# Performance work log

Measured on AMD Instinct MI355X. Metric: run time of the kernel, lower is better.

Reference implementation:

```python
import math
import jax, jax.numpy as jnp
import numpy as np

B, S, H, NH = 4, 2048, 1024, 16
HD = H // NH  # 64


def _rope_cos_sin(seq_len, dim, base=10000.0):
    # freqs[j] = base^(-2j/dim), angles = outer(t, freqs)
    inv = 1.0 / (base ** (jnp.arange(0, dim, 2, dtype=jnp.float32) / dim))
    t = jnp.arange(seq_len, dtype=jnp.float32)
    ang = jnp.outer(t, inv)  # (S, dim//2)
    return jnp.cos(ang), jnp.sin(ang)


def _apply_rope(x, cos, sin):
    # x: (B, S, NH, HD); pairs are (x[2i], x[2i+1]) per torch view_as_complex on reshape(..., -1, 2)
    xr = x.reshape(*x.shape[:-1], HD // 2, 2)
    x0, x1 = xr[..., 0], xr[..., 1]
    c = cos[None, :, None, :]  # (1, S, 1, HD//2)
    s = sin[None, :, None, :]
    o0 = x0 * c - x1 * s
    o1 = x0 * s + x1 * c
    return jnp.stack([o0, o1], axis=-1).reshape(x.shape)


def setup_inputs() -> dict:
    key = jax.random.key(0)
    ks = jax.random.split(key, 5)
    scale = 1.0 / math.sqrt(H)
    return {
        "x": jax.random.normal(ks[0], (B, S, H), dtype=jnp.float32),
        "wq": jax.random.normal(ks[1], (H, H), dtype=jnp.float32) * scale,
        "wk": jax.random.normal(ks[2], (H, H), dtype=jnp.float32) * scale,
        "wv": jax.random.normal(ks[3], (H, H), dtype=jnp.float32) * scale,
        "wo": jax.random.normal(ks[4], (H, H), dtype=jnp.float32) * scale,
        "attention_mask": jnp.ones((B, S), dtype=jnp.int32),
    }


def reference(x, wq, wk, wv, wo, attention_mask):
    # Linear(bias=False): y = x @ W.T with W shape (out, in)
    q = jnp.einsum('bsh,oh->bso', x, wq).reshape(B, S, NH, HD)
    k = jnp.einsum('bsh,oh->bso', x, wk).reshape(B, S, NH, HD)
    v = jnp.einsum('bsh,oh->bso', x, wv).reshape(B, S, NH, HD)
    cos, sin = _rope_cos_sin(S, HD)
    q = _apply_rope(q, cos, sin)
    k = _apply_rope(k, cos, sin)
    # scores: (B, NH, S, S)
    scores = jnp.einsum('bqhd,bkhd->bhqk', q, k) / math.sqrt(HD)
    mask = attention_mask[:, None, None, :]  # (B,1,1,S)
    scores = jnp.where(mask == 0, -jnp.inf, scores)
    attn = jax.nn.softmax(scores, axis=-1)
    # attn_dropout: eval mode / p=0 -> identity
    out = jnp.einsum('bhqk,bkhd->bqhd', attn, v).reshape(B, S, H)
    return jnp.einsum('bsh,oh->bso', out, wo)
```

## Files before the change

### kernel.cpp

```cpp
#include <hip/hip_runtime.h>
#include <hip/hip_bf16.h>

#define B_   4
#define S_   2048
#define H_   1024
#define NH_  16
#define HD_  64
#define M_   8192
#define K_   1024

using bf16x8 = __bf16 __attribute__((ext_vector_type(8)));
using f32x4  = float __attribute__((ext_vector_type(4)));
using f32x16 = float __attribute__((ext_vector_type(16)));

__device__ inline f32x4 mfma16(bf16x8 a, bf16x8 b, f32x4 c) {
    return __builtin_amdgcn_mfma_f32_16x16x32_bf16(a, b, c, 0, 0, 0);
}
__device__ inline f32x16 mfma32(bf16x8 a, bf16x8 b, f32x16 c) {
    return __builtin_amdgcn_mfma_f32_32x32x16_bf16(a, b, c, 0, 0, 0);
}

__device__ inline unsigned short f2bf(float f) {
    __hip_bfloat16 h = __float2bfloat16(f);
    return *reinterpret_cast<unsigned short*>(&h);
}

__device__ inline unsigned cvt_pk_bf16(float lo, float hi) {
    unsigned r;
    asm("v_cvt_pk_bf16_f32 %0, %1, %2" : "=v"(r) : "v"(lo), "v"(hi));
    return r;
}

__device__ inline void perm32swap(unsigned &a, unsigned &b) {
    asm("v_permlane32_swap_b32 %0, %1" : "+v"(a), "+v"(b));
}

__device__ inline void gload_lds16(const unsigned short* g, unsigned short* l) {
    __builtin_amdgcn_global_load_lds(
        (const __attribute__((address_space(1))) void*)g,
        (__attribute__((address_space(3))) void*)l, 16, 0, 0);
}

#define EXP2F(x) __builtin_amdgcn_exp2f(x)


__global__ __launch_bounds__(256) void prep_convert(
    const float* __restrict__ x,  const float* __restrict__ wq,
    const float* __restrict__ wk, const float* __restrict__ wv,
    const float* __restrict__ wo, unsigned short* __restrict__ ws)
{
    size_t u = (size_t)blockIdx.x * 256 + threadIdx.x;
    const float* src; unsigned short* dst; size_t off;
    if (u < 2097152)      { src = x;  dst = ws;            off = u * 4; }
    else if (u < 2359296) { src = wq; dst = ws + 8388608;  off = (u - 2097152) * 4; }
    else if (u < 2621440) { src = wk; dst = ws + 9437184;  off = (u - 2359296) * 4; }
    else if (u < 2883584) { src = wv; dst = ws + 10485760; off = (u - 2621440) * 4; }
    else                  { src = wo; dst = ws + 11534336; off = (u - 2883584) * 4; }
    float4 v = *reinterpret_cast<const float4*>(src + off);
    ushort4 o;
    o.x = f2bf(v.x); o.y = f2bf(v.y); o.z = f2bf(v.z); o.w = f2bf(v.w);
    *reinterpret_cast<ushort4*>(dst + off) = o;
}

__global__ __launch_bounds__(256) void rope_table(
    float* __restrict__ cosb, float* __restrict__ sinb,
    const int* __restrict__ mask, float* __restrict__ biasb)
{
    int idx = blockIdx.x * 256 + threadIdx.x;
    int pos = idx >> 5, i = idx & 31;
    float inv = expf(-(float)(2 * i) * (9.210340371976184f / 64.0f));
    float ang = (float)pos * inv;
    cosb[idx] = cosf(ang);
    sinb[idx] = sinf(ang);
    if (idx < B_ * S_)
        biasb[idx] = mask[idx] ? -12.0f : -__builtin_inff();
}

__global__ __launch_bounds__(256) void gemm_qkv(
    const unsigned short* __restrict__ A,
    const unsigned short* __restrict__ W,
    unsigned short* __restrict__ qbuf, unsigned short* __restrict__ kbuf,
    unsigned short* __restrict__ vtb,
    const float* __restrict__ cosb, const float* __restrict__ sinb)
{
    __shared__ alignas(16) unsigned short Al[128 * 64];
    __shared__ alignas(16) unsigned short Bl[128 * 64];

    const int t = threadIdx.x;
    const int l = t & 63;
    const int w = t >> 6;
    const int lane_r = l & 15, lane_g = l >> 4;
    const int bn = blockIdx.x, bm = blockIdx.y;
    const size_t rowbase = (size_t)bm * 128;
    const int colbase = bn * 128;
    const int wm = (w >> 1) * 64, wn = (w & 1) * 64;
    const int which = colbase >> 10;
    const float scale = (which == 0) ? 0.18033688089184827f : 1.0f;

    const int glrow  = l >> 3;
    const int glslot = (l & 7) ^ glrow;

    f32x4 zero4 = {0.f, 0.f, 0.f, 0.f};
    f32x4 acc[4][4];
#pragma unroll
    for (int a = 0; a < 4; a++)
#pragma unroll
        for (int b2 = 0; b2 < 4; b2++) acc[a][b2] = zero4;

    for (int k0 = 0; k0 < K_; k0 += 64) {
#pragma unroll
        for (int i = 0; i < 4; i++) {
            int rbase = i * 32 + w * 8;
            int row = rbase + glrow;
            gload_lds16(A + (rowbase + row) * K_ + k0 + glslot * 8, &Al[rbase * 64]);
            gload_lds16(W + (size_t)(colbase + row) * K_ + k0 + glslot * 8, &Bl[rbase * 64]);
        }
        __syncthreads();

        bf16x8 af[4][2], bfr[4][2];
#pragma unroll
        for (int mt = 0; mt < 4; mt++)
#pragma unroll
            for (int kk = 0; kk < 2; kk++) {
                int rowa = wm + mt * 16 + lane_r;
                int offa = (rowa * 128 + kk * 64 + lane_g * 16) ^ ((rowa & 7) << 4);
                af[mt][kk] = *reinterpret_cast<const bf16x8*>((const char*)Al + offa);
                int rowb = wn + mt * 16 + lane_r;
                int offb = (rowb * 128 + kk * 64 + lane_g * 16) ^ ((rowb & 7) << 4);
                bfr[mt][kk] = *reinterpret_cast<const bf16x8*>((const char*)Bl + offb);
            }
#pragma unroll
        for (int mt = 0; mt < 4; mt++)
#pragma unroll
            for (int nt = 0; nt < 4; nt++) {
                acc[mt][nt] = mfma16(af[mt][0], bfr[nt][0], acc[mt][nt]);
                acc[mt][nt] = mfma16(af[mt][1], bfr[nt][1], acc[mt][nt]);
            }
        __syncthreads();
    }

#pragma unroll
    for (int mt = 0; mt < 4; mt++) {
#pragma unroll
        for (int nt = 0; nt < 4; nt++) {
            if (which <= 1) {
                unsigned short* out = which ? kbuf : qbuf;
#pragma unroll
                for (int i = 0; i < 4; i++) {
                    size_t r = rowbase + wm + mt * 16 + lane_g * 4 + i;
                    int n = (colbase & 1023) + wn + nt * 16 + lane_r;
                    int b   = (int)(r >> 11);
                    int pos = (int)(r & 2047);
                    int h = n >> 6, d = n & 63;
                    float cv = cosb[pos * 32 + (d >> 1)];
                    float sv = sinb[pos * 32 + (d >> 1)];
                    float val = acc[mt][nt][i];
                    float partner = __shfl_xor(val, 1);
                    float o = (d & 1) ? (partner * sv + val * cv)
                                      : (val * cv - partner * sv);
                    o *= scale;
                    out[(((size_t)(b * NH_ + h)) * S_ + pos) * 64 + d] = f2bf(o);
                }
            } else {
                unsigned short* out = vtb;
                size_t rr = rowbase + wm + mt * 16 + lane_g * 4;
                int n = (colbase & 1023) + wn + nt * 16 + lane_r;
                int b   = (int)(rr >> 11);
                int pos = (int)(rr & 2047);
                int h = n >> 6, d = n & 63;
                ushort4 o;
                o.x = f2bf(acc[mt][nt][0]); o.y = f2bf(acc[mt][nt][1]);
                o.z = f2bf(acc[mt][nt][2]); o.w = f2bf(acc[mt][nt][3]);
                *reinterpret_cast<ushort4*>(
                    out + (((size_t)(b * NH_ + h)) * 64 + d) * S_ + pos) = o;
            }
        }
    }
}

__global__ __launch_bounds__(256) void gemm_wo(
    const unsigned short* __restrict__ A,
    const unsigned short* __restrict__ W,
    float* __restrict__ out)
{
    __shared__ alignas(16) unsigned short Al[128 * 64];
    __shared__ alignas(16) unsigned short Bl[128 * 64];

    const int t = threadIdx.x;
    const int l = t & 63;
    const int w = t >> 6;
    const int lane_r = l & 15, lane_g = l >> 4;
    const int bn = blockIdx.x, bm = blockIdx.y;
    const size_t rowbase = (size_t)bm * 128;
    const int colbase = bn * 128;
    const int wm = (w >> 1) * 64, wn = (w & 1) * 64;

    const int glrow  = l >> 3;
    const int glslot = (l & 7) ^ glrow;

    f32x4 zero4 = {0.f, 0.f, 0.f, 0.f};
    f32x4 acc[4][4];
#pragma unroll
    for (int a = 0; a < 4; a++)
#pragma unroll
        for (int b2 = 0; b2 < 4; b2++) acc[a][b2] = zero4;

    for (int k0 = 0; k0 < K_; k0 += 64) {
#pragma unroll
        for (int i = 0; i < 4; i++) {
            int rbase = i * 32 + w * 8;
            int row = rbase + glrow;
            gload_lds16(A + (rowbase + row) * K_ + k0 + glslot * 8, &Al[rbase * 64]);
            gload_lds16(W + (size_t)(colbase + row) * K_ + k0 + glslot * 8, &Bl[rbase * 64]);
        }
        __syncthreads();

        bf16x8 af[4][2], bfr[4][2];
#pragma unroll
        for (int mt = 0; mt < 4; mt++)
#pragma unroll
            for (int kk = 0; kk < 2; kk++) {
                int rowa = wm + mt * 16 + lane_r;
                int offa = (rowa * 128 + kk * 64 + lane_g * 16) ^ ((rowa & 7) << 4);
                af[mt][kk] = *reinterpret_cast<const bf16x8*>((const char*)Al + offa);
                int rowb = wn + mt * 16 + lane_r;
                int offb = (rowb * 128 + kk * 64 + lane_g * 16) ^ ((rowb & 7) << 4);
                bfr[mt][kk] = *reinterpret_cast<const bf16x8*>((const char*)Bl + offb);
            }
#pragma unroll
        for (int mt = 0; mt < 4; mt++)
#pragma unroll
            for (int nt = 0; nt < 4; nt++) {
                acc[mt][nt] = mfma16(af[mt][0], bfr[nt][0], acc[mt][nt]);
                acc[mt][nt] = mfma16(af[mt][1], bfr[nt][1], acc[mt][nt]);
            }
        __syncthreads();
    }

#pragma unroll
    for (int mt = 0; mt < 4; mt++)
#pragma unroll
        for (int nt = 0; nt < 4; nt++)
#pragma unroll
            for (int i = 0; i < 4; i++) {
                size_t r = rowbase + wm + mt * 16 + lane_g * 4 + i;
                int n = colbase + wn + nt * 16 + lane_r;
                out[r * 1024 + n] = acc[mt][nt][i];
            }
}

__global__ __launch_bounds__(256, 2) void attn_fwd(
    const unsigned short* __restrict__ qb, const unsigned short* __restrict__ kb,
    const unsigned short* __restrict__ vt, const float* __restrict__ biasb,
    unsigned short* __restrict__ ao)
{
    __shared__ alignas(16) unsigned short Kl[2][64 * 64];
    __shared__ alignas(16) unsigned short Vl[2][64 * 64];

    const int bid = blockIdx.x;
    const int xcd = bid & 7, idx = bid >> 3;
    const int bh = xcd * 8 + (idx >> 3);
    const int qt = idx & 7;
    const int b = bh >> 4, h = bh & 15;

    const int t = threadIdx.x, l = t & 63, w = t >> 6;
    const int lr = l & 31;
    const int hi = l >> 5;
    const int row8 = lr & 7;

    const unsigned short* qp = qb + (size_t)bh * S_ * 64;
    const unsigned short* kp = kb + (size_t)bh * S_ * 64;
    const unsigned short* vp = vt + (size_t)bh * 64 * S_;
    const float* bp = biasb + (size_t)b * S_;

    bf16x8 qf[2][4];
#pragma unroll
    for (int qbk = 0; qbk < 2; qbk++) {
        int qrow = qt * 256 + w * 64 + qbk * 32 + lr;
#pragma unroll
        for (int ks = 0; ks < 4; ks++)
            qf[qbk][ks] = *reinterpret_cast<const bf16x8*>(
                qp + (size_t)qrow * 64 + ks * 16 + hi * 8);
    }

    f32x16 oacc[2][2];
#pragma unroll
    for (int qbk = 0; qbk < 2; qbk++)
#pragma unroll
        for (int r = 0; r < 16; r++) { oacc[qbk][0][r] = 0.f; oacc[qbk][1][r] = 0.f; }
    float lsum[2] = {0.f, 0.f};

    const int grr = l >> 3;
    const int gss = ((l & 7) ^ grr) * 8;

#define STAGE(bi, kt)                                                          \
    {                                                                          \
        _Pragma("unroll")                                                      \
        for (int c = 0; c < 2; c++) {                                          \
            int rbase = w * 16 + c * 8;                                        \
            gload_lds16(kp + (size_t)((kt) * 64 + rbase + grr) * 64 + gss,     \
                        &Kl[bi][rbase * 64]);                                  \
            gload_lds16(vp + (size_t)(rbase + grr) * S_ + (kt) * 64 + gss,     \
                        &Vl[bi][rbase * 64]);                                  \
        }                                                                      \
    }

    STAGE(0, 0)

    for (int kt = 0; kt < 32; kt++) {
        const int cur = kt & 1;
        __syncthreads();
        if (kt < 31) STAGE(cur ^ 1, kt + 1)

        f32x16 sacc[2][2];
#pragma unroll
        for (int T = 0; T < 2; T++) {
#pragma unroll
            for (int g = 0; g < 4; g++) {
                float4 bv = *reinterpret_cast<const float4*>(
                    bp + kt * 64 + T * 32 + g * 8 + hi * 4);
                sacc[0][T][g * 4 + 0] = bv.x; sacc[0][T][g * 4 + 1] = bv.y;
                sacc[0][T][g * 4 + 2] = bv.z; sacc[0][T][g * 4 + 3] = bv.w;
            }
            sacc[1][T] = sacc[0][T];
        }

        __builtin_amdgcn_s_setprio(1);
#pragma unroll
        for (int T = 0; T < 2; T++) {
            int rowb = (32 * T + lr) * 128;
#pragma unroll
            for (int ks = 0; ks < 4; ks++) {
                bf16x8 kf = *reinterpret_cast<const bf16x8*>(
                    (const char*)Kl[cur] + rowb + (((2 * ks + hi) ^ row8) << 4));
                sacc[0][T] = mfma32(kf, qf[0][ks], sacc[0][T]);
                sacc[1][T] = mfma32(kf, qf[1][ks], sacc[1][T]);
            }
        }
        __builtin_amdgcn_s_setprio(0);

        bf16x8 pa[2][4];
#pragma unroll
        for (int qbk = 0; qbk < 2; qbk++) {
            unsigned u[2][8];
            float r0 = 0.f, r1 = 0.f, r2 = 0.f, r3 = 0.f;
#pragma unroll
            for (int T = 0; T < 2; T++) {
                float p[16];
#pragma unroll
                for (int r = 0; r < 16; r++) p[r] = EXP2F(sacc[qbk][T][r]);
#pragma unroll
                for (int r = 0; r < 16; r += 4) {
                    r0 += p[r]; r1 += p[r + 1]; r2 += p[r + 2]; r3 += p[r + 3];
                }
#pragma unroll
                for (int bq = 0; bq < 4; bq++) {
                    u[T][bq * 2 + 0] = cvt_pk_bf16(p[bq * 4 + 0], p[bq * 4 + 1]);
                    u[T][bq * 2 + 1] = cvt_pk_bf16(p[bq * 4 + 2], p[bq * 4 + 3]);
                }
            }
            lsum[qbk] += (r0 + r1) + (r2 + r3);
#pragma unroll
            for (int ks = 0; ks < 4; ks++) {
                int T = ks >> 1, e = ks & 1;
                unsigned a0 = u[T][4 * e + 0], b0 = u[T][4 * e + 2];
                unsigned a1 = u[T][4 * e + 1], b1 = u[T][4 * e + 3];
                perm32swap(a0, b0);
                perm32swap(a1, b1);
                unsigned q4[4] = {a0, a1, b0, b1};
                pa[qbk][ks] = *reinterpret_cast<const bf16x8*>(q4);
            }
        }

        __builtin_amdgcn_s_setprio(1);
#pragma unroll
        for (int dt = 0; dt < 2; dt++) {
            int rowb = (32 * dt + lr) * 128;
#pragma unroll
            for (int ks = 0; ks < 4; ks++) {
                bf16x8 vf = *reinterpret_cast<const bf16x8*>(
                    (const char*)Vl[cur] + rowb + (((2 * ks + hi) ^ row8) << 4));
                oacc[0][dt] = mfma32(vf, pa[0][ks], oacc[0][dt]);
                oacc[1][dt] = mfma32(vf, pa[1][ks], oacc[1][dt]);
            }
        }
        __builtin_amdgcn_s_setprio(0);
    }
#undef STAGE

#pragma unroll
    for (int qbk = 0; qbk < 2; qbk++) {
        float ls = lsum[qbk];
        ls += __shfl_xor(ls, 32);
        float rl = 1.0f / ls;
        size_t obase = ((size_t)(b * S_) + qt * 256 + w * 64 + qbk * 32 + lr) * 1024 + h * 64;
#pragma unroll
        for (int dt = 0; dt < 2; dt++)
#pragma unroll
            for (int g = 0; g < 4; g++) {
                uint2 o;
                o.x = cvt_pk_bf16(oacc[qbk][dt][g * 4 + 0] * rl, oacc[qbk][dt][g * 4 + 1] * rl);
                o.y = cvt_pk_bf16(oacc[qbk][dt][g * 4 + 2] * rl, oacc[qbk][dt][g * 4 + 3] * rl);
                *reinterpret_cast<uint2*>(ao + obase + 32 * dt + 8 * g + 4 * hi) = o;
            }
    }
}

extern "C" void kernel_launch(void* const* d_in, const int* in_sizes, int n_in,
                              void* d_out, int out_size, void* d_ws, size_t ws_size,
                              hipStream_t stream)
{
    const float* x  = (const float*)d_in[0];
    const float* wq = (const float*)d_in[1];
    const float* wk = (const float*)d_in[2];
    const float* wv = (const float*)d_in[3];
    const float* wo = (const float*)d_in[4];
    const int* mask = (const int*)d_in[5];

    unsigned short* ws   = (unsigned short*)d_ws;
    unsigned short* xb   = ws;
    unsigned short* wqkv = ws + 8388608;
    unsigned short* wob  = ws + 11534336;
    unsigned short* qbuf = ws + 12582912;
    unsigned short* kbuf = ws + 20971520;
    unsigned short* vtb  = ws + 29360128;
    float* cosb  = (float*)(ws + 37748736);
    float* sinb  = cosb + 65536;
    float* biasb = sinb + 65536;
    unsigned short* aob = xb;

    prep_convert<<<12288, 256, 0, stream>>>(x, wq, wk, wv, wo, ws);
    rope_table<<<256, 256, 0, stream>>>(cosb, sinb, mask, biasb);

    gemm_qkv<<<dim3(24, 64), 256, 0, stream>>>(xb, wqkv, qbuf, kbuf, vtb, cosb, sinb);

    attn_fwd<<<512, 256, 0, stream>>>(qbuf, kbuf, vtb, biasb, aob);

    gemm_wo<<<dim3(8, 64), 256, 0, stream>>>(aob, wob, (float*)d_out);
}
```

Before: 203.7 us.

## Transpose QK MFMA operands for vectorized RoPE epilogue, interleave cos/sin, prefetch bias

```diff
diff --git a/kernel.cpp b/kernel.cpp
--- a/kernel.cpp
+++ b/kernel.cpp
@@ -63,15 +63,15 @@
 }
 
 __global__ __launch_bounds__(256) void rope_table(
-    float* __restrict__ cosb, float* __restrict__ sinb,
-    const int* __restrict__ mask, float* __restrict__ biasb)
+    float2* __restrict__ ropeb, const int* __restrict__ mask,
+    float* __restrict__ biasb)
 {
     int idx = blockIdx.x * 256 + threadIdx.x;
     int pos = idx >> 5, i = idx & 31;
     float inv = expf(-(float)(2 * i) * (9.210340371976184f / 64.0f));
     float ang = (float)pos * inv;
-    cosb[idx] = cosf(ang);
-    sinb[idx] = sinf(ang);
+    float2 cs; cs.x = cosf(ang); cs.y = sinf(ang);
+    ropeb[idx] = cs;
     if (idx < B_ * S_)
         biasb[idx] = mask[idx] ? -12.0f : -__builtin_inff();
 }
@@ -81,7 +81,7 @@
     const unsigned short* __restrict__ W,
     unsigned short* __restrict__ qbuf, unsigned short* __restrict__ kbuf,
     unsigned short* __restrict__ vtb,
-    const float* __restrict__ cosb, const float* __restrict__ sinb)
+    const float* __restrict__ ropeb)
 {
     __shared__ alignas(16) unsigned short Al[128 * 64];
     __shared__ alignas(16) unsigned short Bl[128 * 64];
@@ -129,52 +129,68 @@
                 int offb = (rowb * 128 + kk * 64 + lane_g * 16) ^ ((rowb & 7) << 4);
                 bfr[mt][kk] = *reinterpret_cast<const bf16x8*>((const char*)Bl + offb);
             }
-#pragma unroll
-        for (int mt = 0; mt < 4; mt++)
-#pragma unroll
-            for (int nt = 0; nt < 4; nt++) {
-                acc[mt][nt] = mfma16(af[mt][0], bfr[nt][0], acc[mt][nt]);
-                acc[mt][nt] = mfma16(af[mt][1], bfr[nt][1], acc[mt][nt]);
-            }
+        if (which <= 1) {
+#pragma unroll
+            for (int a = 0; a < 4; a++)
+#pragma unroll
+                for (int b2 = 0; b2 < 4; b2++) {
+                    acc[a][b2] = mfma16(bfr[a][0], af[b2][0], acc[a][b2]);
+                    acc[a][b2] = mfma16(bfr[a][1], af[b2][1], acc[a][b2]);
+                }
+        } else {
+#pragma unroll
+            for (int a = 0; a < 4; a++)
+#pragma unroll
+                for (int b2 = 0; b2 < 4; b2++) {
+                    acc[a][b2] = mfma16(af[a][0], bfr[b2][0], acc[a][b2]);
+                    acc[a][b2] = mfma16(af[a][1], bfr[b2][1], acc[a][b2]);
+                }
+        }
         __syncthreads();
     }
 
-#pragma unroll
-    for (int mt = 0; mt < 4; mt++) {
-#pragma unroll
-        for (int nt = 0; nt < 4; nt++) {
-            if (which <= 1) {
-                unsigned short* out = which ? kbuf : qbuf;
-#pragma unroll
-                for (int i = 0; i < 4; i++) {
-                    size_t r = rowbase + wm + mt * 16 + lane_g * 4 + i;
-                    int n = (colbase & 1023) + wn + nt * 16 + lane_r;
-                    int b   = (int)(r >> 11);
-                    int pos = (int)(r & 2047);
-                    int h = n >> 6, d = n & 63;
-                    float cv = cosb[pos * 32 + (d >> 1)];
-                    float sv = sinb[pos * 32 + (d >> 1)];
-                    float val = acc[mt][nt][i];
-                    float partner = __shfl_xor(val, 1);
-                    float o = (d & 1) ? (partner * sv + val * cv)
-                                      : (val * cv - partner * sv);
-                    o *= scale;
-                    out[(((size_t)(b * NH_ + h)) * S_ + pos) * 64 + d] = f2bf(o);
-                }
-            } else {
-                unsigned short* out = vtb;
-                size_t rr = rowbase + wm + mt * 16 + lane_g * 4;
-                int n = (colbase & 1023) + wn + nt * 16 + lane_r;
-                int b   = (int)(rr >> 11);
+    if (which <= 1) {
+        unsigned short* out = which ? kbuf : qbuf;
+#pragma unroll
+        for (int a = 0; a < 4; a++) {
+            int nbase = (colbase & 1023) + wn + a * 16 + 4 * lane_g;
+            int h = nbase >> 6, d0 = nbase & 63;
+#pragma unroll
+            for (int b2 = 0; b2 < 4; b2++) {
+                size_t r = rowbase + wm + b2 * 16 + lane_r;
+                int bb  = (int)(r >> 11);
+                int pos = (int)(r & 2047);
+                float4 cs = *reinterpret_cast<const float4*>(
+                    ropeb + pos * 64 + d0);
+                float a0 = acc[a][b2][0], a1 = acc[a][b2][1];
+                float a2 = acc[a][b2][2], a3 = acc[a][b2][3];
+                float o0 = (a0 * cs.x - a1 * cs.y) * scale;
+                float o1 = (a0 * cs.y + a1 * cs.x) * scale;
+                float o2 = (a2 * cs.z - a3 * cs.w) * scale;
+                float o3 = (a2 * cs.w + a3 * cs.z) * scale;
+                uint2 o;
+                o.x = cvt_pk_bf16(o0, o1);
+                o.y = cvt_pk_bf16(o2, o3);
+                *reinterpret_cast<uint2*>(
+                    out + (((size_t)(bb * NH_ + h)) * S_ + pos) * 64 + d0) = o;
+            }
+        }
+    } else {
+#pragma unroll
+        for (int a = 0; a < 4; a++)
+#pragma unroll
+            for (int b2 = 0; b2 < 4; b2++) {
+                size_t rr = rowbase + wm + a * 16 + lane_g * 4;
+                int n = (colbase & 1023) + wn + b2 * 16 + lane_r;
+                int bb  = (int)(rr >> 11);
                 int pos = (int)(rr & 2047);
                 int h = n >> 6, d = n & 63;
                 ushort4 o;
-                o.x = f2bf(acc[mt][nt][0]); o.y = f2bf(acc[mt][nt][1]);
-                o.z = f2bf(acc[mt][nt][2]); o.w = f2bf(acc[mt][nt][3]);
+                o.x = f2bf(acc[a][b2][0]); o.y = f2bf(acc[a][b2][1]);
+                o.z = f2bf(acc[a][b2][2]); o.w = f2bf(acc[a][b2][3]);
                 *reinterpret_cast<ushort4*>(
-                    out + (((size_t)(b * NH_ + h)) * 64 + d) * S_ + pos) = o;
-            }
-        }
+                    vtb + (((size_t)(bb * NH_ + h)) * 64 + d) * S_ + pos) = o;
+            }
     }
 }
 
@@ -305,7 +321,19 @@
         }                                                                      \
     }
 
+#define LOADBIAS(kt)                                                           \
+    {                                                                          \
+        _Pragma("unroll")                                                      \
+        for (int T = 0; T < 2; T++)                                            \
+            _Pragma("unroll")                                                  \
+            for (int g = 0; g < 4; g++)                                        \
+                bvreg[T * 4 + g] = *reinterpret_cast<const float4*>(           \
+                    bp + (kt) * 64 + T * 32 + g * 8 + hi * 4);                 \
+    }
+
+    float4 bvreg[8];
     STAGE(0, 0)
+    LOADBIAS(0)
 
     for (int kt = 0; kt < 32; kt++) {
         const int cur = kt & 1;
@@ -314,16 +342,16 @@
 
         f32x16 sacc[2][2];
 #pragma unroll
-        for (int T = 0; T < 2; T++) {
+        for (int T = 0; T < 2; T++)
 #pragma unroll
             for (int g = 0; g < 4; g++) {
-                float4 bv = *reinterpret_cast<const float4*>(
-                    bp + kt * 64 + T * 32 + g * 8 + hi * 4);
+                float4 bv = bvreg[T * 4 + g];
                 sacc[0][T][g * 4 + 0] = bv.x; sacc[0][T][g * 4 + 1] = bv.y;
                 sacc[0][T][g * 4 + 2] = bv.z; sacc[0][T][g * 4 + 3] = bv.w;
-            }
-            sacc[1][T] = sacc[0][T];
-        }
+                sacc[1][T][g * 4 + 0] = bv.x; sacc[1][T][g * 4 + 1] = bv.y;
+                sacc[1][T][g * 4 + 2] = bv.z; sacc[1][T][g * 4 + 3] = bv.w;
+            }
+        if (kt < 31) LOADBIAS(kt + 1)
 
         __builtin_amdgcn_s_setprio(1);
 #pragma unroll
@@ -387,6 +415,7 @@
         __builtin_amdgcn_s_setprio(0);
     }
 #undef STAGE
+#undef LOADBIAS
 
 #pragma unroll
     for (int qbk = 0; qbk < 2; qbk++) {
@@ -424,15 +453,14 @@
     unsigned short* qbuf = ws + 12582912;
     unsigned short* kbuf = ws + 20971520;
     unsigned short* vtb  = ws + 29360128;
-    float* cosb  = (float*)(ws + 37748736);
-    float* sinb  = cosb + 65536;
-    float* biasb = sinb + 65536;
+    float* ropeb = (float*)(ws + 37748736);
+    float* biasb = (float*)(ws + 38010880);
     unsigned short* aob = xb;
 
     prep_convert<<<12288, 256, 0, stream>>>(x, wq, wk, wv, wo, ws);
-    rope_table<<<256, 256, 0, stream>>>(cosb, sinb, mask, biasb);
-
-    gemm_qkv<<<dim3(24, 64), 256, 0, stream>>>(xb, wqkv, qbuf, kbuf, vtb, cosb, sinb);
+    rope_table<<<256, 256, 0, stream>>>((float2*)ropeb, mask, biasb);
+
+    gemm_qkv<<<dim3(24, 64), 256, 0, stream>>>(xb, wqkv, qbuf, kbuf, vtb, ropeb);
 
     attn_fwd<<<512, 256, 0, stream>>>(qbuf, kbuf, vtb, biasb, aob);
 
```

Result: no change. 203.8 us (+0.0%).
